# Performance work log

Hardware: AMD Instinct MI355X
Metric: run time of the kernel (lower is better)

Reference implementation:

```python
import jax, jax.numpy as jnp
import numpy as np

TWN_THRESHOLD_FACTOR = 0.05
BN_EPS = 1e-5


def ternary_quantize(w):
    # threshold = 0.05 * max|w| (detached); q in {-1, 0, +1}
    t = TWN_THRESHOLD_FACTOR * jnp.max(jnp.abs(jax.lax.stop_gradient(w)))
    return (w > t).astype(w.dtype) - (w < -t).astype(w.dtype)


def conv2d(x, w, b):
    q = ternary_quantize(w)
    y = jax.lax.conv_general_dilated(x, q, (1, 1), 'VALID',
                                     dimension_numbers=('NCHW', 'OIHW', 'NCHW'))
    return y + b[None, :, None, None]


def linear(x, w, b):
    q = ternary_quantize(w)
    return x @ q.T + b


def bn_train(x, gamma, beta, axes):
    # training-mode batch norm (biased variance), matches torch BN in train()
    mean = jnp.mean(x, axis=axes, keepdims=True)
    var = jnp.var(x, axis=axes, keepdims=True)
    xhat = (x - mean) * jax.lax.rsqrt(var + BN_EPS)
    shape = [1] * x.ndim
    shape[1] = x.shape[1]
    return xhat * gamma.reshape(shape) + beta.reshape(shape)


def maxpool2(x):
    return jax.lax.reduce_window(x, -jnp.inf, jax.lax.max,
                                 (1, 1, 2, 2), (1, 1, 2, 2), 'VALID')


def setup_inputs() -> dict:
    key = jax.random.key(0)
    ks = jax.random.split(key, 8)
    B, Cin, H, W = 512, 1, 28, 28
    C1, C2, K = 64, 128, 5
    FLAT, F1, F2 = 4 * 4 * C2, 512, 10
    inp = {
        'x': jax.random.normal(ks[0], (B, Cin, H, W), jnp.float32),
        'conv1_w': jax.random.normal(ks[1], (C1, Cin, K, K), jnp.float32) * (1.0 / np.sqrt(Cin * K * K)),
        'conv1_b': jax.random.normal(ks[2], (C1,), jnp.float32) * 0.05,
        'bn1_g': jnp.ones((C1,), jnp.float32),
        'bn1_b': jnp.zeros((C1,), jnp.float32),
        'conv2_w': jax.random.normal(ks[3], (C2, C1, K, K), jnp.float32) * (1.0 / np.sqrt(C1 * K * K)),
        'conv2_b': jax.random.normal(ks[4], (C2,), jnp.float32) * 0.05,
        'bn2_g': jnp.ones((C2,), jnp.float32),
        'bn2_b': jnp.zeros((C2,), jnp.float32),
        'fc1_w': jax.random.normal(ks[5], (F1, FLAT), jnp.float32) * (1.0 / np.sqrt(FLAT)),
        'fc1_b': jax.random.normal(ks[6], (F1,), jnp.float32) * 0.05,
        'bn3_g': jnp.ones((F1,), jnp.float32),
        'bn3_b': jnp.zeros((F1,), jnp.float32),
        'fc2_w': jax.random.normal(ks[7], (F2, F1), jnp.float32) * (1.0 / np.sqrt(F1)),
        'fc2_b': jnp.zeros((F2,), jnp.float32),
    }
    return inp


def reference(x, conv1_w, conv1_b, bn1_g, bn1_b, conv2_w, conv2_b, bn2_g, bn2_b,
              fc1_w, fc1_b, bn3_g, bn3_b, fc2_w, fc2_b):
    h = jax.nn.relu(bn_train(conv2d(x, conv1_w, conv1_b), bn1_g, bn1_b, (0, 2, 3)))
    h = maxpool2(h)  # [B, 64, 12, 12]
    h = jax.nn.relu(bn_train(conv2d(h, conv2_w, conv2_b), bn2_g, bn2_b, (0, 2, 3)))
    h = maxpool2(h)  # [B, 128, 4, 4]
    h = h.reshape(h.shape[0], -1)  # [B, 2048]
    h = jax.nn.relu(bn_train(linear(h, fc1_w, fc1_b), bn3_g, bn3_b, (0,)))
    return linear(h, fc2_w, fc2_b)  # [B, 10]
```

## Files before the change

### kernel.cpp

```cpp
#include <hip/hip_runtime.h>
#include <stdint.h>

#define EPS 1e-5f

typedef short v8s __attribute__((ext_vector_type(8)));
typedef float v4f __attribute__((ext_vector_type(4)));

static const size_t W1F  = 4096;
static const size_t W2F  = 8192;
static const size_t WF2F = 212992;
static const size_t A_F  = 262144;
static const size_t B_F  = 19136512;
static const size_t WF1T = B_F + 1048576;

__device__ inline unsigned short f2bf(float f) {
    unsigned u = __float_as_uint(f);
    return (unsigned short)((u + 0x7FFF + ((u >> 16) & 1)) >> 16);
}

__device__ __forceinline__ void stage16(const unsigned short* g, unsigned short* l) {
    __builtin_amdgcn_global_load_lds(
        (const __attribute__((address_space(1))) unsigned int*)g,
        (__attribute__((address_space(3))) unsigned int*)l, 16, 0, 0);
}

__global__ void k_zero(float* p, int n) {
    int i = blockIdx.x * blockDim.x + threadIdx.x;
    if (i < n) p[i] = 0.f;
}

__global__ void k_absmax4(const float* __restrict__ w0, int n0,
                          const float* __restrict__ w1, int n1,
                          const float* __restrict__ w2, int n2,
                          const float* __restrict__ w3, int n3,
                          float* outv) {
    int blk = blockIdx.x;
    const float* w; int n; unsigned* out; int nb; int bi;
    if (blk < 1)        { w = w0; n = n0; out = (unsigned*)(outv + 0); nb = 1;   bi = blk;      }
    else if (blk < 17)  { w = w1; n = n1; out = (unsigned*)(outv + 1); nb = 16;  bi = blk - 1;  }
    else if (blk < 209) { w = w2; n = n2; out = (unsigned*)(outv + 2); nb = 192; bi = blk - 17; }
    else                { w = w3; n = n3; out = (unsigned*)(outv + 3); nb = 1;   bi = blk - 209; }
    float m = 0.f;
    for (int i = bi * 256 + threadIdx.x; i < n; i += nb * 256)
        m = fmaxf(m, fabsf(w[i]));
    #pragma unroll
    for (int o = 32; o; o >>= 1) m = fmaxf(m, __shfl_down(m, o));
    if ((threadIdx.x & 63) == 0) atomicMax(out, __float_as_uint(m));
}

__global__ void k_quantE(const float* __restrict__ c1w, const float* __restrict__ c2w,
                         const float* __restrict__ f2w, const float* __restrict__ am,
                         float* __restrict__ w1t, unsigned short* __restrict__ w2u,
                         float* __restrict__ wf2) {
    int blk = blockIdx.x;
    if (blk < 1) {
        float t = 0.05f * am[0];
        for (int i = threadIdx.x; i < 1600; i += 256) {
            float v = c1w[i];
            float q = (float)((v > t) - (v < -t));
            int c = i / 25, k = i - c * 25;
            w1t[k * 64 + c] = q;
        }
    } else if (blk < 401) {
        float t = 0.05f * am[1];
        int base = (blk - 1) * 512;
        #pragma unroll
        for (int jj = 0; jj < 2; ++jj) {
            int i = base + jj * 256 + threadIdx.x;
            int j    = i & 7;
            int lane = (i >> 3) & 63;
            int mt   = (i >> 9) & 7;
            int ks   = (i >> 12) & 1;
            int p    = i >> 13;
            int c  = mt * 16 + (lane & 15);
            int ci = ks * 32 + (lane >> 4) * 8 + j;
            float v = c2w[c * 1600 + ci * 25 + p];
            w2u[i] = (v > t) ? (unsigned short)0x3F80
                             : ((v < -t) ? (unsigned short)0xBF80 : (unsigned short)0);
        }
    } else {
        float t = 0.05f * am[3];
        for (int i = threadIdx.x; i < 5120; i += 256) {
            float v = f2w[i];
            wf2[i] = (float)((v > t) - (v < -t));
        }
    }
}

__global__ __launch_bounds__(512) void k_conv1(const float* __restrict__ x,
                                               const float* __restrict__ w1t,
                                               unsigned* __restrict__ pmn1,
                                               float* __restrict__ sum,
                                               float* __restrict__ ssq) {
    __shared__ float xs[784];
    __shared__ float red[2][8][64];
    int b = blockIdx.x;
    const float4* xim = (const float4*)(x + (size_t)b * 784);
    for (int i = threadIdx.x; i < 196; i += 512) ((float4*)xs)[i] = xim[i];
    int c  = threadIdx.x & 63;
    int wv = threadIdx.x >> 6;
    float w[25];
    #pragma unroll
    for (int k = 0; k < 25; ++k) w[k] = w1t[k * 64 + c];
    __syncthreads();
    unsigned* ob = pmn1 + (size_t)b * 9216;
    float s = 0.f, s2 = 0.f;
    int ph = 0, pw = wv;
    for (int it = 0; it < 18; ++it) {
        const float* xp = xs + (ph * 2) * 28 + pw * 2;
        float win[36];
        #pragma unroll
        for (int i = 0; i < 6; ++i)
            #pragma unroll
            for (int j = 0; j < 3; ++j) {
                float2 t2 = *(const float2*)(xp + i * 28 + j * 2);
                win[i * 6 + j * 2] = t2.x; win[i * 6 + j * 2 + 1] = t2.y;
            }
        float v00 = 0.f, v01 = 0.f, v10 = 0.f, v11 = 0.f;
        #pragma unroll
        for (int i = 0; i < 5; ++i)
            #pragma unroll
            for (int j = 0; j < 5; ++j) {
                float wk = w[i * 5 + j];
                v00 = fmaf(win[i * 6 + j],           wk, v00);
                v01 = fmaf(win[i * 6 + j + 1],       wk, v01);
                v10 = fmaf(win[(i + 1) * 6 + j],     wk, v10);
                v11 = fmaf(win[(i + 1) * 6 + j + 1], wk, v11);
            }
        s  += v00 + v01 + v10 + v11;
        s2 += v00 * v00 + v01 * v01 + v10 * v10 + v11 * v11;
        float mx = fmaxf(fmaxf(v00, v01), fmaxf(v10, v11));
        float mn = fminf(fminf(v00, v01), fminf(v10, v11));
        ob[(ph * 12 + pw) * 64 + c] = ((unsigned)f2bf(mx) << 16) | (unsigned)f2bf(mn);
        pw += 8; if (pw >= 12) { pw -= 12; ++ph; }
    }
    red[0][wv][c] = s; red[1][wv][c] = s2;
    __syncthreads();
    if (threadIdx.x < 64) {
        float S = 0.f, S2 = 0.f;
        #pragma unroll
        for (int i = 0; i < 8; ++i) { S += red[0][i][threadIdx.x]; S2 += red[1][i][threadIdx.x]; }
        atomicAdd(&sum[threadIdx.x], S);
        atomicAdd(&ssq[threadIdx.x], S2);
    }
}

__global__ void k_bnpool1(const unsigned* __restrict__ pmn1,
                          const float* __restrict__ c1sum, const float* __restrict__ c1ssq,
                          const float* __restrict__ g1, const float* __restrict__ b1,
                          unsigned short* __restrict__ pool1) {
    int i = blockIdx.x * 256 + threadIdx.x;
    int c = i & 63;
    const float invN = 1.f / 294912.f;
    float mean = c1sum[c] * invN;
    float var  = c1ssq[c] * invN - mean * mean;
    float sc = g1[c] * rsqrtf(var + EPS);
    float sh = b1[c] - mean * sc;
    unsigned u = pmn1[i];
    float mx = __uint_as_float(u & 0xffff0000u);
    float mn = __uint_as_float(u << 16);
    float v = (sc > 0.f) ? mx : mn;
    pool1[i] = f2bf(fmaxf(0.f, fmaf(v, sc, sh)));
}

__global__ __launch_bounds__(256) void k_conv2(const unsigned short* __restrict__ pool1,
                                               const unsigned short* __restrict__ wfrag,
                                               float* __restrict__ pmn,
                                               float* __restrict__ sum,
                                               float* __restrict__ ssq) {
    __shared__ unsigned short xs[144 * 76];
    __shared__ unsigned short wb[2][4096];
    __shared__ float reds[2][64], redq[2][64];
    int b     = blockIdx.x >> 1;
    int mhalf = blockIdx.x & 1;
    int tid  = threadIdx.x;
    int lane = tid & 63;
    int wave = tid >> 6;
    int nh = wave & 1, kp = wave >> 1;
    const unsigned short* src = pool1 + (size_t)b * 9216;
    for (int i = tid; i < 1152; i += 256) {
        int r = i >> 3, part = i & 7;
        *(float4*)(&xs[r * 76 + part * 8]) = *(const float4*)(src + r * 64 + part * 8);
    }
    #pragma unroll
    for (int h = 0; h < 2; ++h) {
        int ksm = wave * 2 + h;
        int ks = ksm >> 2, mt = ksm & 3;
        const unsigned short* g = wfrag + (size_t)(ks * 8 + mhalf * 4 + mt) * 512 + lane * 8;
        stage16(g, &wb[0][ks * 2048 + mt * 512 + lane * 8]);
    }
    __syncthreads();

    int n = lane & 15, quad = lane >> 4;
    int ow = n & 7;
    int ohb0 = nh * 4 + (n >> 3);
    int col0 = kp * 32 + quad * 8;
    v4f acc[4][2];
    #pragma unroll
    for (int mm = 0; mm < 4; ++mm) { acc[mm][0] = (v4f){0,0,0,0}; acc[mm][1] = (v4f){0,0,0,0}; }
    for (int p = 0; p < 25; ++p) {
        int cur = p & 1;
        if (p < 24) {
            #pragma unroll
            for (int h = 0; h < 2; ++h) {
                int ksm = wave * 2 + h;
                int ks = ksm >> 2, mt = ksm & 3;
                const unsigned short* g = wfrag +
                    (size_t)(((p + 1) * 2 + ks) * 8 + mhalf * 4 + mt) * 512 + lane * 8;
                stage16(g, &wb[cur ^ 1][ks * 2048 + mt * 512 + lane * 8]);
            }
        }
        int kh = p / 5, kw = p - (p / 5) * 5;
        int col = (ow + kw) * 76 + col0;
        v8s bf0 = *(const v8s*)(&xs[(ohb0 + kh) * 912 + col]);
        v8s bf1 = *(const v8s*)(&xs[(ohb0 + 2 + kh) * 912 + col]);
        #pragma unroll
        for (int mm = 0; mm < 4; ++mm) {
            v8s af = *(const v8s*)(&wb[cur][kp * 2048 + mm * 512 + lane * 8]);
            acc[mm][0] = __builtin_amdgcn_mfma_f32_16x16x32_bf16(af, bf0, acc[mm][0], 0, 0, 0);
            acc[mm][1] = __builtin_amdgcn_mfma_f32_16x16x32_bf16(af, bf1, acc[mm][1], 0, 0, 0);
        }
        __syncthreads();
    }
    float* mbuf = (float*)xs;
    if (kp == 1) {
        float* d = mbuf + (nh * 64 + lane) * 36;
        #pragma unroll
        for (int mm = 0; mm < 4; ++mm) {
            *(v4f*)(d + mm * 8)     = acc[mm][0];
            *(v4f*)(d + mm * 8 + 4) = acc[mm][1];
        }
    }
    __syncthreads();
    if (kp == 0) {
        const float* s = mbuf + (nh * 64 + lane) * 36;
        #pragma unroll
        for (int mm = 0; mm < 4; ++mm) {
            acc[mm][0] += *(const v4f*)(s + mm * 8);
            acc[mm][1] += *(const v4f*)(s + mm * 8 + 4);
        }
        float* po = pmn + (size_t)b * 4096;
        #pragma unroll
        for (int mm = 0; mm < 4; ++mm) {
            int cl0 = mm * 16 + quad * 4;
            #pragma unroll
            for (int r = 0; r < 4; ++r) {
                int cl = cl0 + r;
                int c  = mhalf * 64 + cl;
                float sA = 0.f, s2A = 0.f;
                #pragma unroll
                for (int bf = 0; bf < 2; ++bf) {
                    float v = acc[mm][bf][r];
                    float pm = fmaxf(v, __shfl_xor(v, 1));
                    float pn = fminf(v, __shfl_xor(v, 1));
                    pm = fmaxf(pm, __shfl_xor(pm, 8));
                    pn = fminf(pn, __shfl_xor(pn, 8));
                    if (((n & 1) == 0) && (n < 8)) {
                        int psp = (nh * 2 + bf) * 4 + (n >> 1);
                        *(float2*)(&po[(c * 16 + psp) * 2]) = make_float2(pm, pn);
                    }
                    float s = v, s2 = v * v;
                    #pragma unroll
                    for (int m = 1; m < 16; m <<= 1) { s += __shfl_xor(s, m); s2 += __shfl_xor(s2, m); }
                    sA += s; s2A += s2;
                }
                if (n == 0) { reds[nh][cl] = sA; redq[nh][cl] = s2A; }
            }
        }
    }
    __syncthreads();
    if (tid < 64) {
        atomicAdd(&sum[mhalf * 64 + tid], reds[0][tid] + reds[1][tid]);
        atomicAdd(&ssq[mhalf * 64 + tid], redq[0][tid] + redq[1][tid]);
    }
}

__global__ void k_prep_fc1(const float* __restrict__ w, const float* __restrict__ am,
                           unsigned short* __restrict__ wf,
                           const float* __restrict__ pmn2, const float* __restrict__ c2sum,
                           const float* __restrict__ c2ssq, const float* __restrict__ g2,
                           const float* __restrict__ b2, unsigned short* __restrict__ xfrag) {
    if (blockIdx.x < 4096) {
        float t = 0.05f * am[2];
        int i = blockIdx.x * 256 + threadIdx.x;
        int f = i >> 11, k = i & 2047;
        float v = w[i];
        unsigned short q = (v > t) ? (unsigned short)0x3F80
                         : ((v < -t) ? (unsigned short)0xBF80 : (unsigned short)0);
        int ft = f >> 4, fm = f & 15;
        int ks = k >> 5, kr = k & 31;
        int lane = (kr >> 3) * 16 + fm;
        wf[((size_t)(ks * 32 + ft) * 64 + lane) * 8 + (kr & 7)] = q;
    } else {
        int i = (blockIdx.x - 4096) * 256 + threadIdx.x;
        int j    = i & 7;
        int lane = (i >> 3) & 63;
        int bt   = (i >> 9) & 31;
        int ks   = i >> 14;
        int b = bt * 16 + (lane & 15);
        int k = ks * 32 + (lane >> 4) * 8 + j;
        int c = k >> 4, psp = k & 15;
        float2 mm = *(const float2*)(&pmn2[((size_t)b * 2048 + c * 16 + psp) * 2]);
        float mean = c2sum[c] * (1.f / 32768.f);
        float var  = c2ssq[c] * (1.f / 32768.f) - mean * mean;
        float sc = g2[c] * rsqrtf(var + EPS);
        float sh = b2[c] - mean * sc;
        float v = (sc > 0.f) ? mm.x : mm.y;
        xfrag[i] = f2bf(fmaxf(0.f, fmaf(v, sc, sh)));
    }
}

__global__ __launch_bounds__(256) void k_fc1(const unsigned short* __restrict__ xfrag,
                                             const unsigned short* __restrict__ wfrag,
                                             float* __restrict__ out,
                                             float* __restrict__ sum,
                                             float* __restrict__ ssq) {
    int lane = threadIdx.x & 63;
    int wave = threadIdx.x >> 6;
    int ft = (blockIdx.x & 7) * 4 + wave;
    int bT = blockIdx.x >> 3;
    v4f acc = (v4f){0.f, 0.f, 0.f, 0.f};
    for (int ks = 0; ks < 64; ++ks) {
        v8s bfrag = *(const v8s*)(xfrag + ((size_t)(ks * 32 + bT) * 64 + lane) * 8);
        v8s afrag = *(const v8s*)(wfrag + ((size_t)(ks * 32 + ft) * 64 + lane) * 8);
        acc = __builtin_amdgcn_mfma_f32_16x16x32_bf16(afrag, bfrag, acc, 0, 0, 0);
    }
    int bb = bT * 16 + (lane & 15);
    int quad = lane >> 4;
    int f0 = ft * 16 + quad * 4;
    *(float4*)(&out[(size_t)bb * 512 + f0]) =
        make_float4(acc[0], acc[1], acc[2], acc[3]);
    #pragma unroll
    for (int r = 0; r < 4; ++r) {
        float s = acc[r], s2 = s * s;
        #pragma unroll
        for (int m = 1; m < 16; m <<= 1) { s += __shfl_xor(s, m); s2 += __shfl_xor(s2, m); }
        if ((lane & 15) == 0) { atomicAdd(&sum[f0 + r], s); atomicAdd(&ssq[f0 + r], s2); }
    }
}

__global__ __launch_bounds__(256) void k_fc2(const float* __restrict__ x,
                                             const float* __restrict__ w,
                                             const float* __restrict__ bias,
                                             const float* __restrict__ fsum,
                                             const float* __restrict__ fssq,
                                             const float* __restrict__ g3,
                                             const float* __restrict__ b3,
                                             float* __restrict__ out) {
    int lane = threadIdx.x & 63;
    int b = blockIdx.x * 4 + (threadIdx.x >> 6);
    float xa[8], sm[8], sq[8], ga[8], ba[8];
    {
        const float4* p;
        p = (const float4*)(x + (size_t)b * 512 + lane * 8);
        *(float4*)xa = p[0]; *(float4*)(xa + 4) = p[1];
        p = (const float4*)(fsum + lane * 8);
        *(float4*)sm = p[0]; *(float4*)(sm + 4) = p[1];
        p = (const float4*)(fssq + lane * 8);
        *(float4*)sq = p[0]; *(float4*)(sq + 4) = p[1];
        p = (const float4*)(g3 + lane * 8);
        *(float4*)ga = p[0]; *(float4*)(ga + 4) = p[1];
        p = (const float4*)(b3 + lane * 8);
        *(float4*)ba = p[0]; *(float4*)(ba + 4) = p[1];
    }
    float h[8];
    #pragma unroll
    for (int e = 0; e < 8; ++e) {
        float mean = sm[e] * (1.f / 512.f);
        float var  = sq[e] * (1.f / 512.f) - mean * mean;
        float sc = ga[e] * rsqrtf(var + EPS);
        float sh = ba[e] - mean * sc;
        h[e] = fmaxf(0.f, fmaf(xa[e], sc, sh));
    }
    #pragma unroll
    for (int j = 0; j < 10; ++j) {
        const float4* wp = (const float4*)(w + j * 512 + lane * 8);
        float4 w0 = wp[0], w1 = wp[1];
        float p = h[0] * w0.x + h[1] * w0.y + h[2] * w0.z + h[3] * w0.w
                + h[4] * w1.x + h[5] * w1.y + h[6] * w1.z + h[7] * w1.w;
        #pragma unroll
        for (int o = 32; o; o >>= 1) p += __shfl_down(p, o);
        if (lane == 0) out[b * 10 + j] = p + bias[j];
    }
}

extern "C" void kernel_launch(void* const* d_in, const int* in_sizes, int n_in,
                              void* d_out, int out_size, void* d_ws, size_t ws_size,
                              hipStream_t stream) {
    const float* x       = (const float*)d_in[0];
    const float* conv1_w = (const float*)d_in[1];
    const float* bn1_g   = (const float*)d_in[3];
    const float* bn1_b   = (const float*)d_in[4];
    const float* conv2_w = (const float*)d_in[5];
    const float* bn2_g   = (const float*)d_in[7];
    const float* bn2_b   = (const float*)d_in[8];
    const float* fc1_w   = (const float*)d_in[9];
    const float* bn3_g   = (const float*)d_in[11];
    const float* bn3_b   = (const float*)d_in[12];
    const float* fc2_w   = (const float*)d_in[13];
    const float* fc2_b   = (const float*)d_in[14];

    float* wsf = (float*)d_ws;

    float* c1_sum = wsf + 16,   * c1_ssq = wsf + 80;
    float* c2_sum = wsf + 272,  * c2_ssq = wsf + 400;
    float* f_sum  = wsf + 1808, * f_ssq  = wsf + 2320;

    float* w1t = wsf + W1F;
    unsigned short* w2u = (unsigned short*)(wsf + W2F);
    float* wf2 = wsf + WF2F;
    unsigned short* wf1 = (unsigned short*)(wsf + WF1T);
    unsigned* PMN1 = (unsigned*)(wsf + A_F);
    float* PMN2 = wsf + A_F;
    float* A    = wsf + A_F;
    unsigned short* pool1 = (unsigned short*)(wsf + B_F);
    unsigned short* xfrag = (unsigned short*)(wsf + B_F);

    k_zero<<<16, 256, 0, stream>>>(wsf, 4096);

    k_absmax4<<<210, 256, 0, stream>>>(conv1_w, 1600, conv2_w, 204800,
                                       fc1_w, 1048576, fc2_w, 5120, wsf);

    k_quantE<<<402, 256, 0, stream>>>(conv1_w, conv2_w, fc2_w, wsf, w1t, w2u, wf2);

    k_conv1<<<512, 512, 0, stream>>>(x, w1t, PMN1, c1_sum, c1_ssq);

    k_bnpool1<<<18432, 256, 0, stream>>>(PMN1, c1_sum, c1_ssq, bn1_g, bn1_b, pool1);

    k_conv2<<<1024, 256, 0, stream>>>(pool1, w2u, PMN2, c2_sum, c2_ssq);

    k_prep_fc1<<<8192, 256, 0, stream>>>(fc1_w, wsf, wf1, PMN2, c2_sum, c2_ssq,
                                         bn2_g, bn2_b, xfrag);

    k_fc1<<<256, 256, 0, stream>>>(xfrag, wf1, A, f_sum, f_ssq);

    k_fc2<<<128, 256, 0, stream>>>(A, wf2, fc2_b, f_sum, f_ssq, bn3_g, bn3_b,
                                   (float*)d_out);
}
```

Baseline: 210.3 us.

## Prefetch conv2 weight fragments into registers instead of LDS double-buffering

In the conv2 MFMA kernel, weight fragments are now loaded directly from global memory into registers through a three-deep software prefetch ring, in a fully unrolled loop. This replaces the LDS double buffer filled by global_load_lds. The change removes the per-iteration __syncthreads and the LDS staging traffic. In exchange it uses more VGPRs, each wave fetches its own fragments from global or L2, and the unrolled code is larger.

```diff
diff --git a/kernel.cpp b/kernel.cpp
--- a/kernel.cpp
+++ b/kernel.cpp
@@ -16,12 +16,6 @@
 __device__ inline unsigned short f2bf(float f) {
     unsigned u = __float_as_uint(f);
     return (unsigned short)((u + 0x7FFF + ((u >> 16) & 1)) >> 16);
-}
-
-__device__ __forceinline__ void stage16(const unsigned short* g, unsigned short* l) {
-    __builtin_amdgcn_global_load_lds(
-        (const __attribute__((address_space(1))) unsigned int*)g,
-        (__attribute__((address_space(3))) unsigned int*)l, 16, 0, 0);
 }
 
 __global__ void k_zero(float* p, int n) {
@@ -169,7 +163,6 @@
                                                float* __restrict__ sum,
                                                float* __restrict__ ssq) {
     __shared__ unsigned short xs[144 * 76];
-    __shared__ unsigned short wb[2][4096];
     __shared__ float reds[2][64], redq[2][64];
     int b     = blockIdx.x >> 1;
     int mhalf = blockIdx.x & 1;
@@ -182,46 +175,37 @@
         int r = i >> 3, part = i & 7;
         *(float4*)(&xs[r * 76 + part * 8]) = *(const float4*)(src + r * 64 + part * 8);
     }
-    #pragma unroll
-    for (int h = 0; h < 2; ++h) {
-        int ksm = wave * 2 + h;
-        int ks = ksm >> 2, mt = ksm & 3;
-        const unsigned short* g = wfrag + (size_t)(ks * 8 + mhalf * 4 + mt) * 512 + lane * 8;
-        stage16(g, &wb[0][ks * 2048 + mt * 512 + lane * 8]);
-    }
-    __syncthreads();
-
     int n = lane & 15, quad = lane >> 4;
     int ow = n & 7;
     int ohb0 = nh * 4 + (n >> 3);
     int col0 = kp * 32 + quad * 8;
+    const unsigned short* wl = wfrag + (size_t)(kp * 8 + mhalf * 4) * 512 + lane * 8;
+    v8s pf[3][4];
+    #pragma unroll
+    for (int s = 0; s < 3; ++s)
+        #pragma unroll
+        for (int mt = 0; mt < 4; ++mt)
+            pf[s][mt] = *(const v8s*)(wl + (size_t)(s * 16 + mt) * 512);
+    __syncthreads();
     v4f acc[4][2];
     #pragma unroll
     for (int mm = 0; mm < 4; ++mm) { acc[mm][0] = (v4f){0,0,0,0}; acc[mm][1] = (v4f){0,0,0,0}; }
+    #pragma unroll
     for (int p = 0; p < 25; ++p) {
-        int cur = p & 1;
-        if (p < 24) {
-            #pragma unroll
-            for (int h = 0; h < 2; ++h) {
-                int ksm = wave * 2 + h;
-                int ks = ksm >> 2, mt = ksm & 3;
-                const unsigned short* g = wfrag +
-                    (size_t)(((p + 1) * 2 + ks) * 8 + mhalf * 4 + mt) * 512 + lane * 8;
-                stage16(g, &wb[cur ^ 1][ks * 2048 + mt * 512 + lane * 8]);
-            }
-        }
         int kh = p / 5, kw = p - (p / 5) * 5;
         int col = (ow + kw) * 76 + col0;
         v8s bf0 = *(const v8s*)(&xs[(ohb0 + kh) * 912 + col]);
         v8s bf1 = *(const v8s*)(&xs[(ohb0 + 2 + kh) * 912 + col]);
         #pragma unroll
         for (int mm = 0; mm < 4; ++mm) {
-            v8s af = *(const v8s*)(&wb[cur][kp * 2048 + mm * 512 + lane * 8]);
+            v8s af = pf[p % 3][mm];
             acc[mm][0] = __builtin_amdgcn_mfma_f32_16x16x32_bf16(af, bf0, acc[mm][0], 0, 0, 0);
             acc[mm][1] = __builtin_amdgcn_mfma_f32_16x16x32_bf16(af, bf1, acc[mm][1], 0, 0, 0);
-        }
-        __syncthreads();
-    }
+            if (p + 3 < 25)
+                pf[p % 3][mm] = *(const v8s*)(wl + (size_t)((p + 3) * 16 + mm) * 512);
+        }
+    }
+    __syncthreads();
     float* mbuf = (float*)xs;
     if (kp == 1) {
         float* d = mbuf + (nh * 64 + lane) * 36;
```

New measurement: 211.6 us. No clear change (+0.6%).
